# Kernel optimization log

Measured on AMD Instinct MI355X. Metric: run time of the kernel, lower is better.

## Reference

```python
import jax, jax.numpy as jnp
import numpy as np

RC = 5.0                 # cutoff radius (init kwarg)
B, M = 128, 256          # structures per batch, atoms per structure
L = 17.2                 # box edge (Angstrom) -> ~0.05 atoms/A^3, ~27 nbrs/atom at rc=5
P = 2_097_152            # fixed max pair count (output padding)


def _pairs(coord):
    """Cell-list candidate generation + radius filter, batched over structures.

    Faithful to the TF CellListNL (no 'cell' / open-boundary path): atoms are
    shifted to the positive octant, binned into cells of edge rc, and candidate
    pairs are atoms of the same structure whose cell bins differ by at most 1 in
    every dimension (the 27-cell stencil). Final pairs satisfy 0 < dist < rc.
    """
    pos = coord - jnp.min(coord, axis=0)                          # [N,3] shift (as in TF code)
    cell = jnp.floor(pos / RC).astype(jnp.int32)                  # [N,3] cell bins
    posb = pos.reshape(B, M, 3)
    cellb = cell.reshape(B, M, 3)
    diff = posb[:, None, :, :] - posb[:, :, None, :]              # [B,M,M,3] = pos_j - pos_i
    sq = jnp.sum(diff * diff, axis=-1)                            # [B,M,M]
    nz = sq > 0.0
    dist = jnp.sqrt(jnp.where(nz, sq, 1.0)) * nz                  # safe norm (0 on diagonal)
    # 27-neighbor-cell stencil == per-axis bin difference in {-1,0,1}
    nbr = jnp.all(jnp.abs(cellb[:, None, :, :] - cellb[:, :, None, :]) <= 1, axis=-1)
    mask = nbr & (dist < RC) & nz                                 # [B,M,M]
    return diff, dist, mask


def setup_inputs() -> dict:
    key = jax.random.key(0)
    coord = jax.random.uniform(key, (B * M, 3), jnp.float32) * L  # atoms in [0,L)^3 per structure
    ind_1 = jnp.repeat(jnp.arange(B, dtype=jnp.int32), M)         # structure index per atom
    return {"coord": coord, "ind_1": ind_1}


def reference(coord, ind_1):
    # ind_1 is encoded structurally: atoms are laid out as B contiguous blocks of M,
    # so same-structure pairing is enforced by the batched [B,M,M] computation.
    diff, dist, mask = _pairs(coord)
    b, i, j = jnp.nonzero(mask, size=P, fill_value=0)             # fixed-size pair list
    valid = mask[b, i, j]                                         # False on padded rows
    d = dist[b, i, j] * valid                                     # [P]
    df = diff[b, i, j] * valid[:, None]                           # [P,3]
    ind_2 = jnp.stack([b * M + i, b * M + j], axis=1) * valid[:, None].astype(jnp.int32)
    return ind_2, d, df
```

## Files before the change

kernel.cpp:

```cpp
#include <hip/hip_runtime.h>
#include <float.h>

#define MM 256
#define PP 2097152
#define NBLK 512
#define GTH (NBLK * 256)
#define CAP 2048
#define SQMAX 24.999996185302734375f

typedef unsigned long long u64;


__device__ inline void wave_min3(float& x, float& y, float& z) {
    #pragma unroll
    for (int off = 32; off > 0; off >>= 1) {
        x = fminf(x, __shfl_xor(x, off, 64));
        y = fminf(y, __shfl_xor(y, off, 64));
        z = fminf(z, __shfl_xor(z, off, 64));
    }
}

__device__ inline void zero_range(float* __restrict__ o, int lo, int hi, int g) {
    int a = (lo + 3) & ~3;
    if (a > hi) a = hi;
    if (g < a - lo) o[lo + g] = 0.0f;
    float4* o4 = reinterpret_cast<float4*>(o);
    const float4 z4 = make_float4(0.f, 0.f, 0.f, 0.f);
    for (int q = (a >> 2) + g; q < (hi >> 2); q += GTH) o4[q] = z4;
}


__global__ void __launch_bounds__(256)
count_k(const float* __restrict__ coord, float* __restrict__ minvec,
        u64* __restrict__ masks, int* __restrict__ bsums) {
    const int b2 = blockIdx.x;
    const int b = b2 >> 2, rblk = b2 & 3;
    const int t = threadIdx.x;
    const int lane = t & 63, w = t >> 6;

    __shared__ float4 tile4[4][65];
    __shared__ float lmin[3][4];
    __shared__ int wsum[4];

    const float4* c4 = reinterpret_cast<const float4*>(coord);
    float mx = FLT_MAX, my = FLT_MAX, mz = FLT_MAX;
    #pragma unroll 4
    for (int k = 0; k < 32; ++k) {
        const int basei = (k * 256 + t) * 3;
        const float4 f0 = c4[basei + 0];
        const float4 f1 = c4[basei + 1];
        const float4 f2 = c4[basei + 2];
        mx = fminf(mx, fminf(fminf(f0.x, f0.w), fminf(f1.z, f2.y)));
        my = fminf(my, fminf(fminf(f0.y, f1.x), fminf(f1.w, f2.z)));
        mz = fminf(mz, fminf(fminf(f0.z, f1.y), fminf(f2.x, f2.w)));
    }
    wave_min3(mx, my, mz);
    if (lane == 0) { lmin[0][w] = mx; lmin[1][w] = my; lmin[2][w] = mz; }
    __syncthreads();
    mx = fminf(fminf(lmin[0][0], lmin[0][1]), fminf(lmin[0][2], lmin[0][3]));
    my = fminf(fminf(lmin[1][0], lmin[1][1]), fminf(lmin[1][2], lmin[1][3]));
    mz = fminf(fminf(lmin[2][0], lmin[2][1]), fminf(lmin[2][2], lmin[2][3]));
    if (b2 == 0 && t == 0) { minvec[0] = mx; minvec[1] = my; minvec[2] = mz; }

    const int ja = b * MM + t;
    tile4[w][lane] = make_float4(__fsub_rn(coord[3 * ja + 0], mx),
                                 __fsub_rn(coord[3 * ja + 1], my),
                                 __fsub_rn(coord[3 * ja + 2], mz), 0.0f);
    __syncthreads();

    const int i_loc = t >> 2, c = t & 3;
    const float4 pi4 = tile4[rblk][i_loc];
    u64 m = 0ULL;
    for (int jj = 0; jj < 64; ++jj) {
        float4 v = tile4[c][jj];
        float dx = __fsub_rn(v.x, pi4.x);
        float dy = __fsub_rn(v.y, pi4.y);
        float dz = __fsub_rn(v.z, pi4.z);
        float sq = __fadd_rn(__fadd_rn(__fmul_rn(dx, dx), __fmul_rn(dy, dy)),
                             __fmul_rn(dz, dz));
        if (sq > 0.0f && sq <= SQMAX) m |= (1ULL << jj);
    }
    masks[b2 * 256 + t] = m;

    int v = __popcll(m);
    #pragma unroll
    for (int off = 32; off > 0; off >>= 1) v += __shfl_xor(v, off, 64);
    if (lane == 0) wsum[w] = v;
    __syncthreads();
    if (t == 0) bsums[b2] = wsum[0] + wsum[1] + wsum[2] + wsum[3];
}

__global__ void __launch_bounds__(256)
write_k(const float* __restrict__ coord, const float* __restrict__ minvec,
        const u64* __restrict__ masks, const int* __restrict__ bsums,
        float* __restrict__ outF) {
    const int b2 = blockIdx.x;
    const int b = b2 >> 2, rblk = b2 & 3;
    const int t = threadIdx.x;
    const int lane = t & 63, w = t >> 6;

    __shared__ float4 tile4[4][65];
    __shared__ int pre[NBLK];
    __shared__ int sTot;
    __shared__ int wsum[4];
    __shared__ float sd[CAP];
    __shared__ float sind[2 * CAP];
    __shared__ float sdf[3 * CAP];

    const float mnx = minvec[0], mny = minvec[1], mnz = minvec[2];
    const int ja = b * MM + t;
    tile4[w][lane] = make_float4(__fsub_rn(coord[3 * ja + 0], mnx),
                                 __fsub_rn(coord[3 * ja + 1], mny),
                                 __fsub_rn(coord[3 * ja + 2], mnz), 0.0f);

    if (w == 0) {
        int v[8]; int s = 0;
        #pragma unroll
        for (int q = 0; q < 8; ++q) { v[q] = bsums[lane * 8 + q]; s += v[q]; }
        int isum = s;
        #pragma unroll
        for (int off = 1; off < 64; off <<= 1) {
            int u = __shfl_up(isum, off, 64);
            if (lane >= off) isum += u;
        }
        int run = isum - s;
        #pragma unroll
        for (int q = 0; q < 8; ++q) { pre[lane * 8 + q] = run; run += v[q]; }
        if (lane == 63) sTot = run;
    }
    __syncthreads();
    const int base = pre[b2];
    const int total = (sTot < PP) ? sTot : PP;

    const u64 mask = masks[b2 * 256 + t];
    const int cnt = __popcll(mask);
    int incl = cnt;
    #pragma unroll
    for (int off = 1; off < 64; off <<= 1) {
        int v = __shfl_up(incl, off, 64);
        if (lane >= off) incl += v;
    }
    if (lane == 63) wsum[w] = incl;
    __syncthreads();
    const int agg = wsum[0] + wsum[1] + wsum[2] + wsum[3];
    int woff = 0;
    for (int k = 0; k < w; ++k) woff += wsum[k];
    const int lexcl = woff + incl - cnt;

    const int i_loc = t >> 2, c = t & 3;
    const float4 pi4 = tile4[rblk][i_loc];
    const int gi = b * MM + rblk * 64 + i_loc;
    const int gj0 = b * MM + c * 64;

    const int nbat = (agg + CAP - 1) / CAP;
    for (int bb = 0; bb < nbat; ++bb) {
        const int wlo = bb * CAP, whi = wlo + CAP;
        int q = lexcl;
        u64 mm = mask;
        while (mm) {
            const int jj = __ffsll((long long)mm) - 1;
            mm &= mm - 1;
            if (q >= whi) break;
            if (q >= wlo) {
                float4 v = tile4[c][jj];
                float dx = __fsub_rn(v.x, pi4.x);
                float dy = __fsub_rn(v.y, pi4.y);
                float dz = __fsub_rn(v.z, pi4.z);
                float sq = __fadd_rn(__fadd_rn(__fmul_rn(dx, dx), __fmul_rn(dy, dy)),
                                     __fmul_rn(dz, dz));
                const int s = q - wlo;
                sd[s] = __fsqrt_rn(sq);
                sind[2 * s + 0] = (float)gi;
                sind[2 * s + 1] = (float)(gj0 + jj);
                sdf[3 * s + 0] = dx;
                sdf[3 * s + 1] = dy;
                sdf[3 * s + 2] = dz;
            }
            q++;
        }
        __syncthreads();
        const int nq = ((agg - wlo) < CAP) ? (agg - wlo) : CAP;
        const int pbase = base + wlo;
        int rem = PP - pbase; if (rem < 0) rem = 0;
        const int nv = (nq < rem) ? nq : rem;
        for (int k = t; k < nv; k += 256)     outF[2 * PP + pbase + k]     = sd[k];
        for (int k = t; k < 2 * nv; k += 256) outF[2 * pbase + k]          = sind[k];
        for (int k = t; k < 3 * nv; k += 256) outF[3 * PP + 3 * pbase + k] = sdf[k];
        __syncthreads();
    }

    const int g = b2 * 256 + t;
    zero_range(outF, 2 * total,          2 * PP, g);
    zero_range(outF, 2 * PP + total,     3 * PP, g);
    zero_range(outF, 3 * PP + 3 * total, 6 * PP, g);
}

extern "C" void kernel_launch(void* const* d_in, const int* in_sizes, int n_in,
                              void* d_out, int out_size, void* d_ws, size_t ws_size,
                              hipStream_t stream) {
    const float* coord = (const float*)d_in[0];
    float* outF = (float*)d_out;

    u64*   masks  = (u64*)d_ws;
    int*   bsums  = (int*)(masks + GTH);
    float* minvec = (float*)(bsums + NBLK);

    count_k<<<NBLK, 256, 0, stream>>>(coord, minvec, masks, bsums);
    write_k<<<NBLK, 256, 0, stream>>>(coord, minvec, masks, bsums, outF);
}
```

Baseline: 31.26 us.

## Halve count kernel blocks and vectorize staged output flush with float4 stores

The count kernel now runs 256 blocks of 512 threads, each covering two row-blocks of a structure. This halves the redundant global-min reduction over all coordinates that every block performs. The write kernel stages results in LDS at an offset that matches the global output alignment, then flushes each plane with aligned float4 stores plus scalar edge handling instead of scalar stores. Costs are extra branching in the flush and fewer, larger blocks in the count kernel.

```diff
diff --git a/kernel.cpp b/kernel.cpp
--- a/kernel.cpp
+++ b/kernel.cpp
@@ -4,6 +4,7 @@
 #define MM 256
 #define PP 2097152
 #define NBLK 512
+#define CBLK 256
 #define GTH (NBLK * 256)
 #define CAP 2048
 #define SQMAX 24.999996185302734375f
@@ -29,24 +30,42 @@
     for (int q = (a >> 2) + g; q < (hi >> 2); q += GTH) o4[q] = z4;
 }
 
-
-__global__ void __launch_bounds__(256)
+__device__ inline void flush_plane(const float* __restrict__ lds, int n, int pad,
+                                   float* __restrict__ gdst, int t) {
+    if (n <= 0) return;
+    const int end = pad + n;
+    const int nb = (end + 3) >> 2;
+    for (int m = t; m < nb; m += 256) {
+        const int lo = m << 2;
+        if (lo >= pad && lo + 4 <= end) {
+            *reinterpret_cast<float4*>(gdst + lo) =
+                *reinterpret_cast<const float4*>(lds + lo);
+        } else {
+            const int a = lo < pad ? pad : lo;
+            const int bmax = (lo + 4 < end) ? (lo + 4) : end;
+            for (int e = a; e < bmax; ++e) gdst[e] = lds[e];
+        }
+    }
+}
+
+
+__global__ void __launch_bounds__(512)
 count_k(const float* __restrict__ coord, float* __restrict__ minvec,
         u64* __restrict__ masks, int* __restrict__ bsums) {
-    const int b2 = blockIdx.x;
-    const int b = b2 >> 2, rblk = b2 & 3;
+    const int cb = blockIdx.x;
+    const int b = cb >> 1, h = cb & 1;
     const int t = threadIdx.x;
     const int lane = t & 63, w = t >> 6;
 
     __shared__ float4 tile4[4][65];
-    __shared__ float lmin[3][4];
-    __shared__ int wsum[4];
+    __shared__ float lmin[3][8];
+    __shared__ int wsum[8];
 
     const float4* c4 = reinterpret_cast<const float4*>(coord);
     float mx = FLT_MAX, my = FLT_MAX, mz = FLT_MAX;
     #pragma unroll 4
-    for (int k = 0; k < 32; ++k) {
-        const int basei = (k * 256 + t) * 3;
+    for (int k = 0; k < 16; ++k) {
+        const int basei = (k * 512 + t) * 3;
         const float4 f0 = c4[basei + 0];
         const float4 f1 = c4[basei + 1];
         const float4 f2 = c4[basei + 2];
@@ -57,18 +76,25 @@
     wave_min3(mx, my, mz);
     if (lane == 0) { lmin[0][w] = mx; lmin[1][w] = my; lmin[2][w] = mz; }
     __syncthreads();
-    mx = fminf(fminf(lmin[0][0], lmin[0][1]), fminf(lmin[0][2], lmin[0][3]));
-    my = fminf(fminf(lmin[1][0], lmin[1][1]), fminf(lmin[1][2], lmin[1][3]));
-    mz = fminf(fminf(lmin[2][0], lmin[2][1]), fminf(lmin[2][2], lmin[2][3]));
-    if (b2 == 0 && t == 0) { minvec[0] = mx; minvec[1] = my; minvec[2] = mz; }
-
-    const int ja = b * MM + t;
-    tile4[w][lane] = make_float4(__fsub_rn(coord[3 * ja + 0], mx),
-                                 __fsub_rn(coord[3 * ja + 1], my),
-                                 __fsub_rn(coord[3 * ja + 2], mz), 0.0f);
-    __syncthreads();
-
-    const int i_loc = t >> 2, c = t & 3;
+    mx = fminf(fminf(fminf(lmin[0][0], lmin[0][1]), fminf(lmin[0][2], lmin[0][3])),
+               fminf(fminf(lmin[0][4], lmin[0][5]), fminf(lmin[0][6], lmin[0][7])));
+    my = fminf(fminf(fminf(lmin[1][0], lmin[1][1]), fminf(lmin[1][2], lmin[1][3])),
+               fminf(fminf(lmin[1][4], lmin[1][5]), fminf(lmin[1][6], lmin[1][7])));
+    mz = fminf(fminf(fminf(lmin[2][0], lmin[2][1]), fminf(lmin[2][2], lmin[2][3])),
+               fminf(fminf(lmin[2][4], lmin[2][5]), fminf(lmin[2][6], lmin[2][7])));
+    if (cb == 0 && t == 0) { minvec[0] = mx; minvec[1] = my; minvec[2] = mz; }
+
+    if (t < 256) {
+        const int ja = b * MM + t;
+        tile4[t >> 6][t & 63] = make_float4(__fsub_rn(coord[3 * ja + 0], mx),
+                                            __fsub_rn(coord[3 * ja + 1], my),
+                                            __fsub_rn(coord[3 * ja + 2], mz), 0.0f);
+    }
+    __syncthreads();
+
+    const int rblk = 2 * h + (t >> 8);
+    const int tt = t & 255;
+    const int i_loc = tt >> 2, c = tt & 3;
     const float4 pi4 = tile4[rblk][i_loc];
     u64 m = 0ULL;
     for (int jj = 0; jj < 64; ++jj) {
@@ -80,14 +106,17 @@
                              __fmul_rn(dz, dz));
         if (sq > 0.0f && sq <= SQMAX) m |= (1ULL << jj);
     }
-    masks[b2 * 256 + t] = m;
+    masks[cb * 512 + t] = m;
 
     int v = __popcll(m);
     #pragma unroll
     for (int off = 32; off > 0; off >>= 1) v += __shfl_xor(v, off, 64);
     if (lane == 0) wsum[w] = v;
     __syncthreads();
-    if (t == 0) bsums[b2] = wsum[0] + wsum[1] + wsum[2] + wsum[3];
+    if (t == 0) {
+        bsums[cb * 2 + 0] = wsum[0] + wsum[1] + wsum[2] + wsum[3];
+        bsums[cb * 2 + 1] = wsum[4] + wsum[5] + wsum[6] + wsum[7];
+    }
 }
 
 __global__ void __launch_bounds__(256)
@@ -103,9 +132,9 @@
     __shared__ int pre[NBLK];
     __shared__ int sTot;
     __shared__ int wsum[4];
-    __shared__ float sd[CAP];
-    __shared__ float sind[2 * CAP];
-    __shared__ float sdf[3 * CAP];
+    __shared__ __align__(16) float sd[CAP + 4];
+    __shared__ __align__(16) float sind[2 * CAP + 4];
+    __shared__ __align__(16) float sdf[3 * CAP + 4];
 
     const float mnx = minvec[0], mny = minvec[1], mnz = minvec[2];
     const int ja = b * MM + t;
@@ -155,6 +184,10 @@
     const int nbat = (agg + CAP - 1) / CAP;
     for (int bb = 0; bb < nbat; ++bb) {
         const int wlo = bb * CAP, whi = wlo + CAP;
+        const int pbase = base + wlo;
+        const int pd = pbase & 3;
+        const int pi = (2 * pbase) & 3;
+        const int pf = (3 * pbase) & 3;
         int q = lexcl;
         u64 mm = mask;
         while (mm) {
@@ -169,23 +202,22 @@
                 float sq = __fadd_rn(__fadd_rn(__fmul_rn(dx, dx), __fmul_rn(dy, dy)),
                                      __fmul_rn(dz, dz));
                 const int s = q - wlo;
-                sd[s] = __fsqrt_rn(sq);
-                sind[2 * s + 0] = (float)gi;
-                sind[2 * s + 1] = (float)(gj0 + jj);
-                sdf[3 * s + 0] = dx;
-                sdf[3 * s + 1] = dy;
-                sdf[3 * s + 2] = dz;
+                sd[s + pd] = __fsqrt_rn(sq);
+                sind[2 * s + pi + 0] = (float)gi;
+                sind[2 * s + pi + 1] = (float)(gj0 + jj);
+                sdf[3 * s + pf + 0] = dx;
+                sdf[3 * s + pf + 1] = dy;
+                sdf[3 * s + pf + 2] = dz;
             }
             q++;
         }
         __syncthreads();
         const int nq = ((agg - wlo) < CAP) ? (agg - wlo) : CAP;
-        const int pbase = base + wlo;
         int rem = PP - pbase; if (rem < 0) rem = 0;
         const int nv = (nq < rem) ? nq : rem;
-        for (int k = t; k < nv; k += 256)     outF[2 * PP + pbase + k]     = sd[k];
-        for (int k = t; k < 2 * nv; k += 256) outF[2 * pbase + k]          = sind[k];
-        for (int k = t; k < 3 * nv; k += 256) outF[3 * PP + 3 * pbase + k] = sdf[k];
+        flush_plane(sd,   nv,     pd, outF + 2 * PP + pbase - pd,     t);
+        flush_plane(sind, 2 * nv, pi, outF + 2 * pbase - pi,          t);
+        flush_plane(sdf,  3 * nv, pf, outF + 3 * PP + 3 * pbase - pf, t);
         __syncthreads();
     }
 
@@ -205,6 +237,6 @@
     int*   bsums  = (int*)(masks + GTH);
     float* minvec = (float*)(bsums + NBLK);
 
-    count_k<<<NBLK, 256, 0, stream>>>(coord, minvec, masks, bsums);
+    count_k<<<CBLK, 512, 0, stream>>>(coord, minvec, masks, bsums);
     write_k<<<NBLK, 256, 0, stream>>>(coord, minvec, masks, bsums, outF);
 }
```

Result: faster. 29.01 us (-7.2%).
